# Kernel optimization log

Hardware: AMD Instinct MI355X
Metric: run time of the kernel (lower is better)

## Reference

```python
import jax, jax.numpy as jnp
import numpy as np
from jax import lax

B, T, V, E, H, K = 64, 512, 50002, 300, 256, 11
START, STOP = 9, 10


def _lstm_dir(x, w_ih, w_hh, b, reverse):
    """Single-direction LSTM. x: [B,T,D]; w_ih: [4H,D]; w_hh: [4H,H]; b: [4H]."""
    xw = jnp.einsum('btd,gd->btg', x, w_ih) + b  # precompute input projections [B,T,4H]
    h0 = jnp.zeros((x.shape[0], w_hh.shape[1]), x.dtype)

    def step(carry, xt):
        h, c = carry
        g = xt + h @ w_hh.T                      # [B,4H], gate order i,f,g,o (PyTorch)
        i, f, gg, o = jnp.split(g, 4, axis=-1)
        c = jax.nn.sigmoid(f) * c + jax.nn.sigmoid(i) * jnp.tanh(gg)
        h = jax.nn.sigmoid(o) * jnp.tanh(c)
        return (h, c), h

    _, hs = lax.scan(step, (h0, h0), jnp.swapaxes(xw, 0, 1), reverse=reverse)
    return jnp.swapaxes(hs, 0, 1)  # [B,T,H]


def _bilstm_feats(sentence, emb, fc_w, fc_b,
                  w_ih_l0f, w_hh_l0f, b_l0f, w_ih_l0b, w_hh_l0b, b_l0b,
                  w_ih_l1f, w_hh_l1f, b_l1f, w_ih_l1b, w_hh_l1b, b_l1b):
    x = emb[sentence]  # [B,T,E] (frozen embedding lookup)
    h0 = jnp.concatenate([
        _lstm_dir(x, w_ih_l0f, w_hh_l0f, b_l0f, False),
        _lstm_dir(x, w_ih_l0b, w_hh_l0b, b_l0b, True)], axis=-1)  # [B,T,2H]
    h1 = jnp.concatenate([
        _lstm_dir(h0, w_ih_l1f, w_hh_l1f, b_l1f, False),
        _lstm_dir(h0, w_ih_l1b, w_hh_l1b, b_l1b, True)], axis=-1)  # [B,T,2H]
    return h1 @ fc_w.T + fc_b  # emission scores [B,T,K] (dropout = identity in eval)


def _viterbi(feats, transitions):
    """feats: [B,T,K]; transitions[to, from]: [K,K]. Returns (path_score [B,1], path [B,T])."""
    Bs = feats.shape[0]
    init = jnp.full((Bs, K), -1000.0, feats.dtype).at[:, START].set(0.0)

    def step(fv, feat_t):
        scores = fv[:, None, :] + transitions[None, :, :]  # [B, next, prev]
        best_prev = jnp.argmax(scores, axis=2)             # [B,K]
        vit = jnp.max(scores, axis=2)                      # [B,K]
        return vit + feat_t, best_prev

    fv, bptrs = lax.scan(step, init, jnp.swapaxes(feats, 0, 1))  # bptrs: [T,B,K]
    terminal = fv + transitions[STOP]                             # [B,K]
    path_score = jnp.max(terminal, axis=1, keepdims=True)         # [B,1]
    last_tag = jnp.argmax(terminal, axis=1)                       # [B]

    def back(tag, bp):
        prev = jnp.take_along_axis(bp, tag[:, None], axis=1)[:, 0]
        return prev, prev

    _, prev_tags = lax.scan(back, last_tag, bptrs, reverse=True)  # prev_tags[t] = tag at t-1
    path = jnp.concatenate([prev_tags[1:], last_tag[None]], axis=0)  # [T,B]; drop START
    return path_score, jnp.swapaxes(path, 0, 1)


def setup_inputs() -> dict:
    key = jax.random.key(0)
    ks = jax.random.split(key, 24)
    s = 1.0 / np.sqrt(H)
    inp = {
        'sentence': jax.random.randint(ks[0], (B, T), 0, V, dtype=jnp.int32),
        'batch_lengths': jnp.full((B,), T, dtype=jnp.int32),
        'emb': jax.random.normal(ks[1], (V, E), jnp.float32) * 0.1,
        'fc_w': jax.random.normal(ks[2], (K, 2 * H), jnp.float32) * s,
        'fc_b': jnp.zeros((K,), jnp.float32),
    }
    trans = jax.random.normal(ks[3], (K, K), jnp.float32)
    inp['transitions'] = trans.at[START, :].set(-100000.0).at[:, STOP].set(-100000.0)
    i = 4
    for layer, din in ((0, E), (1, 2 * H)):
        for d in ('f', 'b'):
            inp[f'w_ih_l{layer}{d}'] = jax.random.normal(ks[i], (4 * H, din), jnp.float32) * s
            inp[f'w_hh_l{layer}{d}'] = jax.random.normal(ks[i + 1], (4 * H, H), jnp.float32) * s
            inp[f'b_l{layer}{d}'] = jax.random.normal(ks[i + 2], (4 * H,), jnp.float32) * s
            i += 3
    return inp


def reference(sentence, batch_lengths, emb, fc_w, fc_b, transitions,
              w_ih_l0f, w_hh_l0f, b_l0f, w_ih_l0b, w_hh_l0b, b_l0b,
              w_ih_l1f, w_hh_l1f, b_l1f, w_ih_l1b, w_hh_l1b, b_l1b):
    feats = _bilstm_feats(sentence, emb, fc_w, fc_b,
                          w_ih_l0f, w_hh_l0f, b_l0f, w_ih_l0b, w_hh_l0b, b_l0b,
                          w_ih_l1f, w_hh_l1f, b_l1f, w_ih_l1b, w_hh_l1b, b_l1b)
    score, path = _viterbi(feats, transitions)
    return score, path
```

## Files before the change

### kernel.cpp

```cpp
#include <hip/hip_runtime.h>
#include <cstddef>
#include <cstdint>
#include <math.h>


__device__ __forceinline__ float sigmf_(float x){ return 1.0f/(1.0f+expf(-x)); }

__global__ void k_zero(float* __restrict__ p, int n){
  for (int i = blockIdx.x*blockDim.x + threadIdx.x; i < n; i += gridDim.x*blockDim.x) p[i] = 0.f;
}

__global__ void k_gather(const int* __restrict__ sent, const float* __restrict__ emb,
                         float4* __restrict__ X, int b0, int t0, int logT, int Tm1, int total){
  int idx = blockIdx.x*256 + threadIdx.x;
  if (idx >= total) return;
  int m = idx / 76, k4 = idx - m*76;
  int bl = m >> logT, t = m & Tm1;
  float4 v = make_float4(0.f,0.f,0.f,0.f);
  if (k4 < 75) v = ((const float4*)emb)[(size_t)sent[(size_t)(b0+bl)*512 + t0 + t]*75 + k4];
  X[idx] = v;
}

__global__ void k_prepw(const float* __restrict__ w, float* __restrict__ wT, int din, int dinPad){
  int total = dinPad*1024;
  for (int idx = blockIdx.x*blockDim.x + threadIdx.x; idx < total; idx += gridDim.x*blockDim.x){
    int k = idx >> 10, n = idx & 1023;
    wT[idx] = (k < din) ? w[n*din + k] : 0.f;
  }
}

__global__ __launch_bounds__(256) void k_gemm2(
    const float* __restrict__ A0, const float* __restrict__ A1, int lda, int kTiles,
    int aBstride, int sOff0, int sOff1, int logT, int Tm1,
    const float* __restrict__ B0, const float* __restrict__ B1,
    const float* __restrict__ bias0, const float* __restrict__ bias1,
    float* __restrict__ C0, float* __restrict__ C1){
  __shared__ float As[16][132];
  __shared__ float Bs[16][132];
  const int z = blockIdx.z;
  const float* A   = z ? A1 : A0;
  const float* Bm  = z ? B1 : B0;
  const float* bias= z ? bias1 : bias0;
  float* Cc        = z ? C1 : C0;
  const int sOff   = z ? sOff1 : sOff0;
  const int t  = threadIdx.x;
  const int tx = t & 15, ty = t >> 4;
  const int m0 = blockIdx.y * 128, n0 = blockIdx.x * 128;
  const int arow = t >> 2, ak = (t & 3) * 4;
  const int brow = t >> 5, bc = (t & 31) * 4;
  const int gm0 = m0 + arow, gm1 = m0 + arow + 64;
  const size_t r0 = (size_t)(gm0 >> logT)*aBstride + sOff + (gm0 & Tm1);
  const size_t r1 = (size_t)(gm1 >> logT)*aBstride + sOff + (gm1 & Tm1);
  float acc[8][8] = {};
  for (int kt = 0; kt < kTiles; ++kt){
    const int kb = kt * 16;
    float4 a0 = *(const float4*)(A + r0*lda + kb + ak);
    float4 a1 = *(const float4*)(A + r1*lda + kb + ak);
    float4 b0 = *(const float4*)(Bm + (size_t)(kb+brow)*1024 + n0 + bc);
    float4 b1 = *(const float4*)(Bm + (size_t)(kb+brow+8)*1024 + n0 + bc);
    __syncthreads();
    As[ak+0][arow] = a0.x; As[ak+1][arow] = a0.y; As[ak+2][arow] = a0.z; As[ak+3][arow] = a0.w;
    As[ak+0][arow+64] = a1.x; As[ak+1][arow+64] = a1.y; As[ak+2][arow+64] = a1.z; As[ak+3][arow+64] = a1.w;
    *(float4*)&Bs[brow  ][bc] = b0;
    *(float4*)&Bs[brow+8][bc] = b1;
    __syncthreads();
    #pragma unroll
    for (int k = 0; k < 16; ++k){
      float av[8], bv[8];
      *(float4*)&av[0] = *(const float4*)&As[k][ty*8];
      *(float4*)&av[4] = *(const float4*)&As[k][ty*8+4];
      *(float4*)&bv[0] = *(const float4*)&Bs[k][tx*8];
      *(float4*)&bv[4] = *(const float4*)&Bs[k][tx*8+4];
      #pragma unroll
      for (int i = 0; i < 8; ++i)
        #pragma unroll
        for (int jj = 0; jj < 8; ++jj)
          acc[i][jj] = fmaf(av[i], bv[jj], acc[i][jj]);
    }
  }
  float bvals[8];
  *(float4*)&bvals[0] = *(const float4*)(bias + n0 + tx*8);
  *(float4*)&bvals[4] = *(const float4*)(bias + n0 + tx*8 + 4);
  float* Cp = Cc + (size_t)(m0 + ty*8)*1024 + n0 + tx*8;
  #pragma unroll
  for (int i = 0; i < 8; ++i){
    float4 o0 = make_float4(acc[i][0]+bvals[0], acc[i][1]+bvals[1], acc[i][2]+bvals[2], acc[i][3]+bvals[3]);
    float4 o1 = make_float4(acc[i][4]+bvals[4], acc[i][5]+bvals[5], acc[i][6]+bvals[6], acc[i][7]+bvals[7]);
    *(float4*)(Cp + (size_t)i*1024)     = o0;
    *(float4*)(Cp + (size_t)i*1024 + 4) = o1;
  }
}

__global__ __launch_bounds__(512, 2) void k_lstm2s(
    const float* __restrict__ xwF, const float* __restrict__ xwB,
    const float* __restrict__ whhf, const float* __restrict__ whhb,
    float* __restrict__ hout, int hBstride, int tOffF, int tOffB,
    int T, int epoch,
    float* __restrict__ hx, int* __restrict__ flags,
    float* __restrict__ hsave, float* __restrict__ csave)
{
  __shared__ float hfull[256];
  __shared__ float gls[512];
  __shared__ float wtail[512*66];
  const int blk = blockIdx.x;
  const int hh = (blk >> 3) & 1;
  const int chain = (blk & 7) | ((blk >> 4) << 3);
  const int b_local = chain >> 1;
  const int dir = chain & 1;
  const int t = threadIdx.x;
  const int gateK = t >> 7, i0 = t & 127;
  float4 wL[24], wR[24];
  {
    const float* whh = dir ? whhb : whhf;
    const float* base = whh + (size_t)(gateK*256 + hh*128 + i0)*256;
    const float* a = base + hh*128;
    const float* b = base + (1-hh)*128;
    #pragma unroll
    for (int q = 0; q < 24; ++q){ wL[q] = *(const float4*)(a + q*4); wR[q] = *(const float4*)(b + q*4); }
    for (int q = 24; q < 32; ++q){
      #pragma unroll
      for (int e = 0; e < 4; ++e){
        wtail[t*66 + (q-24)*4 + e]      = a[q*4 + e];
        wtail[t*66 + 32 + (q-24)*4 + e] = b[q*4 + e];
      }
    }
  }
  if (t < 256) hfull[t] = hsave[chain*256 + t];
  float c = (t < 128) ? csave[chain*256 + hh*128 + t] : 0.f;
  __syncthreads();
  const int xcol = gateK*256 + hh*128 + i0;
  const float* xb = (dir ? xwB : xwF) + (size_t)b_local*T*1024 + xcol;
  float* hxme        = hx + (size_t)(chain*2 + hh)*256;
  const float* hxpt  = hx + (size_t)(chain*2 + (1-hh))*256;
  int* flg  = flags + (chain*2 + hh)*16;
  int* flgp = flags + (chain*2 + (1-hh))*16;
  const int tOff = dir ? tOffB : tOffF;
  float* hob = hout + (size_t)b_local*hBstride + dir*256 + hh*128;
  const float* wtb = &wtail[t*66];
  const float4* hL4 = ((const float4*)hfull) + hh*32;
  const float4* hR4 = ((const float4*)hfull) + (1-hh)*32;
  float xg = xb[(size_t)(dir ? (T-1) : 0)*1024];
  float hrem = 0.f;
  for (int s = 0; s < T; ++s){
    const int tt = dir ? (T-1-s) : s;
    float xn = 0.f;
    if (s < T-1) xn = xb[(size_t)(dir ? (T-2-s) : (s+1))*1024];
    if (s > 0 && t < 128) hfull[(1-hh)*128 + t] = hrem;
    float pa = 0.f;
    #pragma unroll
    for (int q = 0; q < 24; ++q){
      float4 hv = hL4[q];
      pa = fmaf(wL[q].x, hv.x, pa);
      pa = fmaf(wL[q].y, hv.y, pa);
      pa = fmaf(wL[q].z, hv.z, pa);
      pa = fmaf(wL[q].w, hv.w, pa);
    }
    #pragma unroll
    for (int q = 24; q < 32; ++q){
      float4 hv = hL4[q];
      const int o = (q-24)*4;
      pa = fmaf(wtb[o+0], hv.x, pa);
      pa = fmaf(wtb[o+1], hv.y, pa);
      pa = fmaf(wtb[o+2], hv.z, pa);
      pa = fmaf(wtb[o+3], hv.w, pa);
    }
    __syncthreads();
    float pb = 0.f;
    #pragma unroll
    for (int q = 0; q < 24; ++q){
      float4 hv = hR4[q];
      pb = fmaf(wR[q].x, hv.x, pb);
      pb = fmaf(wR[q].y, hv.y, pb);
      pb = fmaf(wR[q].z, hv.z, pb);
      pb = fmaf(wR[q].w, hv.w, pb);
    }
    #pragma unroll
    for (int q = 24; q < 32; ++q){
      float4 hv = hR4[q];
      const int o = (q-24)*4;
      pb = fmaf(wtb[32+o+0], hv.x, pb);
      pb = fmaf(wtb[32+o+1], hv.y, pb);
      pb = fmaf(wtb[32+o+2], hv.z, pb);
      pb = fmaf(wtb[32+o+3], hv.w, pb);
    }
    float acc = (pa + pb) + xg;
    float act = (gateK == 2) ? tanhf(acc) : sigmf_(acc);
    gls[t] = act;
    __syncthreads();
    float hval = 0.f;
    if (t < 128){
      c = gls[128 + t]*c + gls[t]*gls[256 + t];
      hval = gls[384 + t]*tanhf(c);
      hfull[hh*128 + t] = hval;
      __hip_atomic_store(&hxme[(s & 1)*128 + t], hval,
                         __ATOMIC_RELAXED, __HIP_MEMORY_SCOPE_AGENT);
    }
    __syncthreads();
    if (t == 0)
      __hip_atomic_store(flg, epoch + s + 1, __ATOMIC_RELAXED, __HIP_MEMORY_SCOPE_AGENT);
    if (t < 128){
      hob[(size_t)(tOff + tt)*512 + t] = hval;
      if (s < T-1){
        int lim = 0;
        while (__hip_atomic_load(flgp, __ATOMIC_RELAXED, __HIP_MEMORY_SCOPE_AGENT) < epoch + s + 1
               && ++lim < (1<<20)) {}
        hrem = __hip_atomic_load(&hxpt[(s & 1)*128 + t],
                                 __ATOMIC_RELAXED, __HIP_MEMORY_SCOPE_AGENT);
      }
    }
    xg = xn;
  }
  if (t < 128){
    hsave[chain*256 + hh*128 + t] = hfull[hh*128 + t];
    csave[chain*256 + hh*128 + t] = c;
  }
}

__global__ __launch_bounds__(256) void k_feats_half(
    const float* __restrict__ h1s, const float* __restrict__ fcw, const float* __restrict__ fcb,
    float* __restrict__ feats, int b0, int logT, int Tm1, int tG0, int dir){
  int wv = threadIdx.x >> 6, lane = threadIdx.x & 63;
  int m = blockIdx.x*4 + wv;
  const float4* row = (const float4*)(h1s + (size_t)m*512 + dir*256);
  float4 rv = row[lane];
  int bl = m >> logT, tl = m & Tm1;
  size_t fbase = ((size_t)(b0 + bl)*512 + tG0 + tl)*11;
  #pragma unroll
  for (int n = 0; n < 11; ++n){
    const float4* wr = (const float4*)(fcw + n*512 + dir*256);
    float4 w4 = wr[lane];
    float p = rv.x*w4.x + rv.y*w4.y + rv.z*w4.z + rv.w*w4.w;
    #pragma unroll
    for (int off = 32; off > 0; off >>= 1) p += __shfl_down(p, off, 64);
    if (lane == 0){
      float add = (dir == 0) ? (p + fcb[n]) : p;
      feats[fbase + n] += add;
    }
  }
}

__global__ __launch_bounds__(256) void k_viterbi(const float* __restrict__ feats,
                        const float* __restrict__ trans, float* __restrict__ out){
  __shared__ unsigned char bp[4][512][12];
  const int wave = threadIdx.x >> 6, lane = threadIdx.x & 63;
  const int b = blockIdx.x*4 + wave;
  const int j = lane;
  float tr[11];
  float fv;
  if (j < 11){
    #pragma unroll
    for (int p = 0; p < 11; ++p) tr[p] = trans[j*11 + p];
    fv = (j == 9) ? 0.f : -1000.f;
  } else {
    #pragma unroll
    for (int p = 0; p < 11; ++p) tr[p] = -1e30f;
    fv = -1e30f;
  }
  for (int t = 0; t < 512; ++t){
    float best = -1e38f; int bestp = 0;
    #pragma unroll
    for (int p = 0; p < 11; ++p){
      float v = __shfl(fv, p, 64) + tr[p];
      if (v > best){ best = v; bestp = p; }
    }
    float feat = (j < 11) ? feats[((size_t)b*512 + t)*11 + j] : 0.f;
    fv = best + feat;
    if (j < 11) bp[wave][t][j] = (unsigned char)bestp;
  }
  float term = (j < 11) ? fv + trans[10*11 + j] : -1e38f;
  float best = -1e38f; int bestp = 0;
  #pragma unroll
  for (int p = 0; p < 11; ++p){
    float v = __shfl(term, p, 64);
    if (v > best){ best = v; bestp = p; }
  }
  if (lane == 0){
    out[b] = best;
    float* path = out + 64 + (size_t)b*512;
    int cur = bestp;
    path[511] = (float)cur;
    for (int t = 511; t >= 1; --t){
      cur = bp[wave][t][cur];
      path[t-1] = (float)cur;
    }
  }
}

extern "C" void kernel_launch(void* const* d_in, const int* in_sizes, int n_in,
                              void* d_out, int out_size, void* d_ws, size_t ws_size,
                              hipStream_t stream){
  const int*   sent  = (const int*)d_in[0];
  const float* emb   = (const float*)d_in[2];
  const float* fcw   = (const float*)d_in[3];
  const float* fcb   = (const float*)d_in[4];
  const float* trans = (const float*)d_in[5];
  const float* wih0f = (const float*)d_in[6];
  const float* whh0f = (const float*)d_in[7];
  const float* b0f   = (const float*)d_in[8];
  const float* wih0b = (const float*)d_in[9];
  const float* whh0b = (const float*)d_in[10];
  const float* b0b   = (const float*)d_in[11];
  const float* wih1f = (const float*)d_in[12];
  const float* whh1f = (const float*)d_in[13];
  const float* b1f   = (const float*)d_in[14];
  const float* wih1b = (const float*)d_in[15];
  const float* whh1b = (const float*)d_in[16];
  const float* b1b   = (const float*)d_in[17];

  float* ws = (float*)d_ws;
  const size_t o_wT0f = 0;
  const size_t o_wT0b = o_wT0f + 311296;
  const size_t o_wT1f = o_wT0b + 311296;
  const size_t o_wT1b = o_wT1f + 524288;
  const size_t o_hx   = o_wT1b + 524288;
  const size_t o_flag = o_hx   + 65536;
  const size_t o_hs   = o_flag + 4096;
  const size_t o_cs   = o_hs   + 32768;
  const size_t o_feat = o_cs   + 32768;
  const size_t o_var  = o_feat + 360448;
  float* wT0f = ws + o_wT0f;
  float* wT0b = ws + o_wT0b;
  float* wT1f = ws + o_wT1f;
  float* wT1b = ws + o_wT1b;
  float* hx    = ws + o_hx;
  int*   flags = (int*)(ws + o_flag);
  float* hsave = ws + o_hs;
  float* csave = ws + o_cs;
  float* feats = ws + o_feat;

  int C = 8, T = 32, logT = 5;
  {
    const int cc[8]  = {64, 64, 32, 32, 16, 16, 8, 8};
    const int tt[8]  = {32, 16, 32, 16, 32, 16, 64, 32};
    const int lt[8]  = { 5,  4,  5,  4,  5,  4,  6,  5};
    for (int i = 0; i < 8; ++i){
      size_t need = (o_var + (size_t)cc[i]*tt[i]*2656 + (size_t)cc[i]*262144)*4;
      if (need <= ws_size){ C = cc[i]; T = tt[i]; logT = lt[i]; break; }
    }
  }
  const int Tm1 = T - 1, S = 512 / T;
  float* XF  = ws + o_var;
  float* XB  = XF + (size_t)C*T*304;
  float* xwF = XB + (size_t)C*T*304;
  float* xwB = xwF + (size_t)C*T*1024;
  float* h0  = xwB + (size_t)C*T*1024;
  float* h1s = XF;

  hipLaunchKernelGGL(k_prepw, dim3(512), dim3(256), 0, stream, wih0f, wT0f, 300, 304);
  hipLaunchKernelGGL(k_prepw, dim3(512), dim3(256), 0, stream, wih0b, wT0b, 300, 304);
  hipLaunchKernelGGL(k_prepw, dim3(512), dim3(256), 0, stream, wih1f, wT1f, 512, 512);
  hipLaunchKernelGGL(k_prepw, dim3(512), dim3(256), 0, stream, wih1b, wT1b, 512, 512);
  hipLaunchKernelGGL(k_zero,  dim3(512), dim3(256), 0, stream, feats, 360448);

  for (int b0 = 0; b0 < 64; b0 += C){
    for (int layer = 0; layer < 2; ++layer){
      hipLaunchKernelGGL(k_zero, dim3(256), dim3(256), 0, stream, ws + o_hx, 65536 + 4096 + 65536);
      const float* whF = layer ? whh1f : whh0f;
      const float* whB = layer ? whh1b : whh0b;
      for (int sl = 0; sl < S; ++sl){
        const int sF = sl, sB = S - 1 - sl;
        const int M = C*T;
        if (layer == 0){
          int total = C*T*76;
          hipLaunchKernelGGL(k_gather, dim3((total+255)/256), dim3(256), 0, stream,
                             sent, emb, (float4*)XF, b0, sF*T, logT, Tm1, total);
          hipLaunchKernelGGL(k_gather, dim3((total+255)/256), dim3(256), 0, stream,
                             sent, emb, (float4*)XB, b0, sB*T, logT, Tm1, total);
          hipLaunchKernelGGL(k_gemm2, dim3(8, M/128, 2), dim3(256), 0, stream,
                             XF, XB, 304, 19, T, 0, 0, logT, Tm1,
                             wT0f, wT0b, b0f, b0b, xwF, xwB);
        } else {
          hipLaunchKernelGGL(k_gemm2, dim3(8, M/128, 2), dim3(256), 0, stream,
                             h0, h0, 512, 32, 512, sF*T, sB*T, logT, Tm1,
                             wT1f, wT1b, b1f, b1b, xwF, xwB);
        }
        {
          const float *xF = xwF, *xB = xwB, *wF = whF, *wB = whB;
          float* hop = layer ? h1s : h0;
          int hBs  = layer ? T*512 : 512*512;
          int tOF  = layer ? 0 : sF*T;
          int tOB  = layer ? 0 : sB*T;
          int Tk = T, ep = sl*T;
          float *hxp = hx, *hsp = hsave, *csp = csave; int *flp = flags;
          void* args[] = {(void*)&xF, (void*)&xB, (void*)&wF, (void*)&wB,
                          (void*)&hop, (void*)&hBs, (void*)&tOF, (void*)&tOB,
                          (void*)&Tk, (void*)&ep,
                          (void*)&hxp, (void*)&flp, (void*)&hsp, (void*)&csp};
          hipLaunchCooperativeKernel((const void*)k_lstm2s, dim3(C*4), dim3(512), args, 0, stream);
        }
        if (layer == 1){
          hipLaunchKernelGGL(k_feats_half, dim3(C*T/4), dim3(256), 0, stream,
                             h1s, fcw, fcb, feats, b0, logT, Tm1, sF*T, 0);
          hipLaunchKernelGGL(k_feats_half, dim3(C*T/4), dim3(256), 0, stream,
                             h1s, fcw, fcb, feats, b0, logT, Tm1, sB*T, 1);
        }
      }
    }
  }
  hipLaunchKernelGGL(k_viterbi, dim3(16), dim3(256), 0, stream, feats, trans, (float*)d_out);
}
```

Before: 6.707 ms.

## Single-thread flag spin, 64-bit h exchange, prefetch Viterbi feats, larger chunk

The LSTM recurrence kernel now has only thread 0 spin on the partner block's flag, and 64 threads fetch the partner's hidden half as 64-bit atomic loads instead of 128 threads each spinning and loading a float. The Viterbi loop is unrolled by four with emission scores prefetched several steps ahead, so global load latency sits off the serial dependency chain. A larger time-chunk option (C=64, T=64) is tried first when the workspace allows it, and the launch bound is rewritten as an explicit waves-per-EU attribute. The single-thread spin relies on the following workgroup barrier for ordering. With relaxed atomics and no fence, the other threads may read stale partner values.

```diff
diff --git a/kernel.cpp b/kernel.cpp
--- a/kernel.cpp
+++ b/kernel.cpp
@@ -91,7 +91,8 @@
   }
 }
 
-__global__ __launch_bounds__(512, 2) void k_lstm2s(
+__global__ __launch_bounds__(512) __attribute__((amdgpu_waves_per_eu(2, 2)))
+void k_lstm2s(
     const float* __restrict__ xwF, const float* __restrict__ xwB,
     const float* __restrict__ whhf, const float* __restrict__ whhb,
     float* __restrict__ hout, int hBstride, int tOffF, int tOffB,
@@ -140,12 +141,15 @@
   const float4* hL4 = ((const float4*)hfull) + hh*32;
   const float4* hR4 = ((const float4*)hfull) + (1-hh)*32;
   float xg = xb[(size_t)(dir ? (T-1) : 0)*1024];
-  float hrem = 0.f;
+  float2 hrem = make_float2(0.f, 0.f);
   for (int s = 0; s < T; ++s){
     const int tt = dir ? (T-1-s) : s;
     float xn = 0.f;
     if (s < T-1) xn = xb[(size_t)(dir ? (T-2-s) : (s+1))*1024];
-    if (s > 0 && t < 128) hfull[(1-hh)*128 + t] = hrem;
+    if (s > 0 && t < 64){
+      hfull[(1-hh)*128 + 2*t]     = hrem.x;
+      hfull[(1-hh)*128 + 2*t + 1] = hrem.y;
+    }
     float pa = 0.f;
     #pragma unroll
     for (int q = 0; q < 24; ++q){
@@ -198,14 +202,18 @@
     __syncthreads();
     if (t == 0)
       __hip_atomic_store(flg, epoch + s + 1, __ATOMIC_RELAXED, __HIP_MEMORY_SCOPE_AGENT);
-    if (t < 128){
-      hob[(size_t)(tOff + tt)*512 + t] = hval;
-      if (s < T-1){
+    if (t < 128) hob[(size_t)(tOff + tt)*512 + t] = hval;
+    if (s < T-1){
+      if (t == 0){
         int lim = 0;
         while (__hip_atomic_load(flgp, __ATOMIC_RELAXED, __HIP_MEMORY_SCOPE_AGENT) < epoch + s + 1
                && ++lim < (1<<20)) {}
-        hrem = __hip_atomic_load(&hxpt[(s & 1)*128 + t],
+      }
+      if (t < 64){
+        union { unsigned long long u; float2 f; } uu;
+        uu.u = __hip_atomic_load((const unsigned long long*)(hxpt + (s & 1)*128 + 2*t),
                                  __ATOMIC_RELAXED, __HIP_MEMORY_SCOPE_AGENT);
+        hrem = uu.f;
       }
     }
     xg = xn;
@@ -256,17 +264,27 @@
     for (int p = 0; p < 11; ++p) tr[p] = -1e30f;
     fv = -1e30f;
   }
-  for (int t = 0; t < 512; ++t){
-    float best = -1e38f; int bestp = 0;
-    #pragma unroll
-    for (int p = 0; p < 11; ++p){
-      float v = __shfl(fv, p, 64) + tr[p];
-      if (v > best){ best = v; bestp = p; }
-    }
-    float feat = (j < 11) ? feats[((size_t)b*512 + t)*11 + j] : 0.f;
-    fv = best + feat;
-    if (j < 11) bp[wave][t][j] = (unsigned char)bestp;
-  }
+  const float* fb = feats + ((size_t)b*512)*11 + j;
+  float f0 = (j < 11) ? fb[0*11] : 0.f;
+  float f1 = (j < 11) ? fb[1*11] : 0.f;
+  float f2 = (j < 11) ? fb[2*11] : 0.f;
+  float f3 = (j < 11) ? fb[3*11] : 0.f;
+#define VSTEP(TT, FREG) {                                            \
+    float best = -1e38f; int bestp = 0;                              \
+    _Pragma("unroll")                                                \
+    for (int p = 0; p < 11; ++p){                                    \
+      float v = __shfl(fv, p, 64) + tr[p];                           \
+      if (v > best){ best = v; bestp = p; }                          \
+    }                                                                \
+    fv = best + FREG;                                                \
+    if (j < 11) bp[wave][TT][j] = (unsigned char)bestp; }
+  for (int t = 0; t < 512; t += 4){
+    VSTEP(t+0, f0); f0 = (j < 11 && t+4 < 512) ? fb[(size_t)(t+4)*11] : 0.f;
+    VSTEP(t+1, f1); f1 = (j < 11 && t+5 < 512) ? fb[(size_t)(t+5)*11] : 0.f;
+    VSTEP(t+2, f2); f2 = (j < 11 && t+6 < 512) ? fb[(size_t)(t+6)*11] : 0.f;
+    VSTEP(t+3, f3); f3 = (j < 11 && t+7 < 512) ? fb[(size_t)(t+7)*11] : 0.f;
+  }
+#undef VSTEP
   float term = (j < 11) ? fv + trans[10*11 + j] : -1e38f;
   float best = -1e38f; int bestp = 0;
   #pragma unroll
@@ -330,10 +348,10 @@
 
   int C = 8, T = 32, logT = 5;
   {
-    const int cc[8]  = {64, 64, 32, 32, 16, 16, 8, 8};
-    const int tt[8]  = {32, 16, 32, 16, 32, 16, 64, 32};
-    const int lt[8]  = { 5,  4,  5,  4,  5,  4,  6,  5};
-    for (int i = 0; i < 8; ++i){
+    const int cc[9]  = {64, 64, 64, 32, 32, 16, 16, 8, 8};
+    const int tt[9]  = {64, 32, 16, 32, 16, 32, 16, 64, 32};
+    const int lt[9]  = { 6,  5,  4,  5,  4,  5,  4,  6,  5};
+    for (int i = 0; i < 9; ++i){
       size_t need = (o_var + (size_t)cc[i]*tt[i]*2656 + (size_t)cc[i]*262144)*4;
       if (need <= ws_size){ C = cc[i]; T = tt[i]; logT = lt[i]; break; }
     }
```

Result: faster. 5.635 ms (-16.0%).
